# Optimization experiments

Hardware: AMD Instinct MI355X
Metric: run time of the kernel (lower is better)

The kernel has to match this reference:

```python
import jax, jax.numpy as jnp
import numpy as np

OS = 14            # output_size
GRID = 2           # ceil(roi_size/OS) = ceil(28/14) = 2 (boxes are built 28x28, sampling_ratio=-1)
NODES = OS * OS    # 196 graph nodes
EPS = 1e-5         # BatchNorm eps
K, B, C, H, W = 256, 4, 256, 112, 112


def _bn_relu(x, g, b, m, v):
    # eval-mode BatchNorm2d followed by ReLU (bn_act_conv prefix)
    s = jax.lax.rsqrt(v + EPS)
    xn = (x - m[None, :, None, None]) * s[None, :, None, None]
    return jax.nn.relu(xn * g[None, :, None, None] + b[None, :, None, None])


def _conv(x, w, b, pad):
    y = jax.lax.conv_general_dilated(x, w, (1, 1), [(pad, pad), (pad, pad)],
                                     dimension_numbers=('NCHW', 'OIHW', 'NCHW'))
    return y + b[None, :, None, None]


def _roi_align(sem, boxes):
    # torchvision roi_align, spatial_scale=1.0, aligned=False, sampling_ratio=-1 (static grid=2)
    Bs, Cc, Hh, Ww = sem.shape
    bidx = boxes[:, 0].astype(jnp.int32)
    x1, y1, x2, y2 = boxes[:, 1], boxes[:, 2], boxes[:, 3], boxes[:, 4]
    bw = jnp.maximum(x2 - x1, 1.0) / OS
    bh = jnp.maximum(y2 - y1, 1.0) / OS
    t = (jnp.arange(OS * GRID, dtype=sem.dtype) + 0.5) / GRID   # pw*GRID+ix collapsed
    xs = x1[:, None] + bw[:, None] * t                          # [K, 28]
    ys = y1[:, None] + bh[:, None] * t

    def prep(c, L):
        m = (c >= -1.0) & (c <= L)
        cc = jnp.clip(c, 0.0, L - 1)
        lo = jnp.floor(cc).astype(jnp.int32)
        hi = jnp.minimum(lo + 1, L - 1)
        return m, lo, hi, cc - lo

    my, yl, yh, ly = prep(ys, Hh)
    mx, xl, xh, lx = prep(xs, Ww)
    semt = jnp.transpose(sem, (0, 2, 3, 1))  # [B,H,W,C]

    def gat(ya, xa):
        return semt[bidx[:, None, None], ya[:, :, None], xa[:, None, :]]  # [K,28,28,C]

    ly_ = ly[:, :, None, None]
    lx_ = lx[:, None, :, None]
    val = (gat(yl, xl) * (1 - ly_) * (1 - lx_) + gat(yl, xh) * (1 - ly_) * lx_
           + gat(yh, xl) * ly_ * (1 - lx_) + gat(yh, xh) * ly_ * lx_)
    val = jnp.where((my[:, :, None] & mx[:, None, :])[..., None], val, 0.0)
    val = val.reshape(-1, OS, GRID, OS, GRID, Cc).mean(axis=(2, 4))  # avg over sampling grid
    return jnp.transpose(val, (0, 3, 1, 2))  # [K,C,14,14]


def _gcn_agg(A, x):
    # PyG gcn_norm on a fully-connected weighted graph (self loops already present):
    # deg[j] = sum_i A[i,j] (scatter on col); out[j] = sum_i d^-1/2[i] A[i,j] d^-1/2[j] x[i]
    deg = A.sum(axis=1)                 # [K,196]
    dis = jax.lax.rsqrt(deg)            # sigmoid weights > 0 => no zero degree
    Nrm = dis[:, :, None] * A * dis[:, None, :]
    return jnp.einsum('kij,kif->kjf', Nrm, x)


def _forward(roi_feature, semantic, boxes,
             bn_sem_g, bn_sem_b, bn_sem_m, bn_sem_v, conv_sem_w, conv_sem_b,
             bn_fpn_g, bn_fpn_b, bn_fpn_m, bn_fpn_v, conv_fpn_w, conv_fpn_b,
             bn_aff_g, bn_aff_b, bn_aff_m, bn_aff_v, conv_aff_w, conv_aff_b,
             gcn1_w, gcn1_b, gcn2_w, gcn2_b):
    roi_sem = _roi_align(semantic, boxes)                                   # [K,256,14,14]
    a = (_conv(_bn_relu(roi_sem, bn_sem_g, bn_sem_b, bn_sem_m, bn_sem_v), conv_sem_w, conv_sem_b, 1)
         + _conv(_bn_relu(roi_feature, bn_fpn_g, bn_fpn_b, bn_fpn_m, bn_fpn_v), conv_fpn_w, conv_fpn_b, 1))
    aff = _conv(_bn_relu(a, bn_aff_g, bn_aff_b, bn_aff_m, bn_aff_v), conv_aff_w, conv_aff_b, 0)
    A = jax.nn.sigmoid(aff.reshape(-1, NODES, NODES))                       # [K,196,196]
    X = roi_feature.reshape(-1, C, NODES).transpose(0, 2, 1)                # [K,196,256] node feats
    x1 = jax.nn.relu(_gcn_agg(A, X @ gcn1_w) + gcn1_b)                      # GCNConv(256,16)+ReLU
    x2 = _gcn_agg(A, x1 @ gcn2_w) + gcn2_b                                  # GCNConv(16,256)
    emb = x2.transpose(0, 2, 1).reshape(-1, C, OS, OS)
    return roi_sem + emb


def setup_inputs() -> dict:
    key = jax.random.key(0)
    ks = jax.random.split(key, 24)
    roi_feature = jax.random.normal(ks[0], (K, C, OS, OS), jnp.float32)
    semantic = jax.random.normal(ks[1], (B, C, H, W), jnp.float32)
    bidx = jax.random.randint(ks[2], (K,), 0, B).astype(jnp.float32)
    xy = jax.random.uniform(ks[3], (K, 2), jnp.float32, 0.0, float(H - 28))
    boxes = jnp.concatenate([bidx[:, None], xy, xy + 28.0], axis=1)  # (idx,x1,y1,x2,y2), 28x28 boxes

    def bn(kg, c):
        k1, k2, k3, k4 = jax.random.split(kg, 4)
        return (jax.random.normal(k1, (c,)) * 0.1 + 1.0,
                jax.random.normal(k2, (c,)) * 0.1,
                jax.random.normal(k3, (c,)) * 0.1,
                jax.random.uniform(k4, (c,), jnp.float32, 0.5, 1.5))
    bn_sem = bn(ks[4], C); bn_fpn = bn(ks[5], C); bn_aff = bn(ks[6], 64)
    inp = {
        'roi_feature': roi_feature, 'semantic': semantic, 'boxes': boxes,
        'bn_sem_g': bn_sem[0], 'bn_sem_b': bn_sem[1], 'bn_sem_m': bn_sem[2], 'bn_sem_v': bn_sem[3],
        'conv_sem_w': jax.random.normal(ks[7], (64, C, 3, 3)) * 0.02,
        'conv_sem_b': jax.random.normal(ks[8], (64,)) * 0.02,
        'bn_fpn_g': bn_fpn[0], 'bn_fpn_b': bn_fpn[1], 'bn_fpn_m': bn_fpn[2], 'bn_fpn_v': bn_fpn[3],
        'conv_fpn_w': jax.random.normal(ks[9], (64, C, 3, 3)) * 0.02,
        'conv_fpn_b': jax.random.normal(ks[10], (64,)) * 0.02,
        'bn_aff_g': bn_aff[0], 'bn_aff_b': bn_aff[1], 'bn_aff_m': bn_aff[2], 'bn_aff_v': bn_aff[3],
        'conv_aff_w': jax.random.normal(ks[11], (NODES, 64, 1, 1)) * 0.05,
        'conv_aff_b': jax.random.normal(ks[12], (NODES,)) * 0.05,
        'gcn1_w': jax.random.normal(ks[13], (C, 16)) * 0.05,
        'gcn1_b': jax.random.normal(ks[14], (16,)) * 0.05,
        'gcn2_w': jax.random.normal(ks[15], (16, C)) * 0.05,
        'gcn2_b': jax.random.normal(ks[16], (C,)) * 0.05,
    }
    return inp


def reference(roi_feature, semantic, boxes,
              bn_sem_g, bn_sem_b, bn_sem_m, bn_sem_v, conv_sem_w, conv_sem_b,
              bn_fpn_g, bn_fpn_b, bn_fpn_m, bn_fpn_v, conv_fpn_w, conv_fpn_b,
              bn_aff_g, bn_aff_b, bn_aff_m, bn_aff_v, conv_aff_w, conv_aff_b,
              gcn1_w, gcn1_b, gcn2_w, gcn2_b):
    return _forward(roi_feature, semantic, boxes,
                    bn_sem_g, bn_sem_b, bn_sem_m, bn_sem_v, conv_sem_w, conv_sem_b,
                    bn_fpn_g, bn_fpn_b, bn_fpn_m, bn_fpn_v, conv_fpn_w, conv_fpn_b,
                    bn_aff_g, bn_aff_b, bn_aff_m, bn_aff_v, conv_aff_w, conv_aff_b,
                    gcn1_w, gcn1_b, gcn2_w, gcn2_b)
```

## Files before the change

kernel.cpp:

```cpp
#include <hip/hip_runtime.h>
#include <hip/hip_bf16.h>

#define KBOX 256
#define CCH  256
#define NODES 196
#define OS 14

typedef __attribute__((ext_vector_type(8))) short  bf16x8;
typedef __attribute__((ext_vector_type(8))) unsigned short u16x8;
typedef __attribute__((ext_vector_type(4))) float  f32x4;
typedef __attribute__((ext_vector_type(4))) short  s16x4;
typedef __attribute__((ext_vector_type(4))) int    i32x4;

__device__ __forceinline__ short f2bf(float x) {
  __hip_bfloat16 h = __float2bfloat16(x);
  return *reinterpret_cast<short*>(&h);
}
__device__ __forceinline__ float bf2f(unsigned short u) {
  unsigned int x = ((unsigned int)u) << 16;
  union { unsigned int i; float f; } c; c.i = x;
  return c.f;
}

#define MFMA16 __builtin_amdgcn_mfma_f32_16x16x32_bf16

__global__ __launch_bounds__(256) void prep_kernel(
    const float* __restrict__ bn_sem_g, const float* __restrict__ bn_sem_b,
    const float* __restrict__ bn_sem_m, const float* __restrict__ bn_sem_v,
    const float* __restrict__ conv_sem_w, const float* __restrict__ conv_sem_b,
    const float* __restrict__ bn_fpn_g, const float* __restrict__ bn_fpn_b,
    const float* __restrict__ bn_fpn_m, const float* __restrict__ bn_fpn_v,
    const float* __restrict__ conv_fpn_w, const float* __restrict__ conv_fpn_b,
    const float* __restrict__ bn_aff_g, const float* __restrict__ bn_aff_b,
    const float* __restrict__ bn_aff_m, const float* __restrict__ bn_aff_v,
    const float* __restrict__ conv_aff_w, const float* __restrict__ g1w,
    const float* __restrict__ g2w,
    float* __restrict__ ss_sem, float* __restrict__ ss_fpn, float* __restrict__ ss_aff2,
    short* __restrict__ wfrag, short* __restrict__ wafrag, short* __restrict__ g1wf,
    short* __restrict__ g2wf)
{
  int gid = blockIdx.x * blockDim.x + threadIdx.x;
  int gsz = gridDim.x * blockDim.x;
  for (int c = gid; c < 256; c += gsz) {
    float s = bn_sem_g[c] * rsqrtf(bn_sem_v[c] + 1e-5f);
    ss_sem[c] = s; ss_sem[256 + c] = bn_sem_b[c] - bn_sem_m[c] * s;
    float s2 = bn_fpn_g[c] * rsqrtf(bn_fpn_v[c] + 1e-5f);
    ss_fpn[c] = s2; ss_fpn[256 + c] = bn_fpn_b[c] - bn_fpn_m[c] * s2;
  }
  for (int c = gid; c < 64; c += gsz) {
    float s = bn_aff_g[c] * rsqrtf(bn_aff_v[c] + 1e-5f);
    float sh = bn_aff_b[c] - bn_aff_m[c] * s;
    float bias = conv_sem_b[c] + conv_fpn_b[c];
    ss_aff2[c] = s; ss_aff2[64 + c] = bias * s + sh;
  }
  for (int idx = gid; idx < 144 * 4 * 64 * 8; idx += gsz) {
    int e = idx & 7, lane = (idx >> 3) & 63, nt = (idx >> 9) & 3, kstep = idx >> 11;
    int src = kstep / 72, rem = kstep % 72, icc = rem / 9, pos = rem % 9;
    int ky = pos / 3, kx = pos % 3;
    int oc = nt * 16 + (lane & 15);
    int ic = icc * 32 + (lane >> 4) * 8 + e;
    const float* w = src ? conv_fpn_w : conv_sem_w;
    wfrag[idx] = f2bf(w[((oc * 256 + ic) * 3 + ky) * 3 + kx]);
  }
  for (int idx = gid; idx < 2 * 13 * 64 * 8; idx += gsz) {
    int t = idx;
    int e = t & 7; t >>= 3;
    int lane = t & 63; t >>= 6;
    int nt = t % 13; int s = t / 13;
    int i = nt * 16 + (lane & 15);
    int ic = s * 32 + (lane >> 4) * 8 + e;
    wafrag[idx] = f2bf(i < NODES ? conv_aff_w[i * 64 + ic] : 0.f);
  }
  for (int idx = gid; idx < 8 * 64 * 8; idx += gsz) {
    int e = idx & 7, lane = (idx >> 3) & 63, ks = idx >> 9;
    int ic = ks * 32 + (lane >> 4) * 8 + e;
    int f = lane & 15;
    g1wf[idx] = f2bf(g1w[ic * 16 + f]);
  }
  for (int idx = gid; idx < 16 * 64 * 8; idx += gsz) {
    int e = idx & 7, lane = (idx >> 3) & 63, ct = idx >> 9;
    int kk = (lane >> 4) * 8 + e;
    int c = ct * 16 + (lane & 15);
    g2wf[idx] = f2bf(kk < 16 ? g2w[kk * 256 + c] : 0.f);
  }
}

__global__ __launch_bounds__(256) void transpose_bf16_kernel(
    const float* __restrict__ in, unsigned short* __restrict__ out, int C, int HW)
{
  __shared__ float tile[64][65];
  int nh = (HW + 63) >> 6;
  int bi = blockIdx.x;
  int cb = bi % (C >> 6); bi /= (C >> 6);
  int hb = bi % nh; int b = bi / nh;
  int tx = threadIdx.x & 63, ty = threadIdx.x >> 6;
  const float* inb = in + (size_t)b * C * HW;
  unsigned short* outb = out + (size_t)b * HW * C;
  #pragma unroll
  for (int i = ty; i < 64; i += 4) {
    int c = cb * 64 + i, hw = hb * 64 + tx;
    tile[i][tx] = (hw < HW) ? inb[(size_t)c * HW + hw] : 0.f;
  }
  __syncthreads();
  int cp = threadIdx.x & 31;
  #pragma unroll
  for (int i = (int)(threadIdx.x >> 5); i < 64; i += 8) {
    int hw = hb * 64 + i;
    if (hw < HW) {
      ushort2 v;
      v.x = (unsigned short)f2bf(tile[cp * 2][i]);
      v.y = (unsigned short)f2bf(tile[cp * 2 + 1][i]);
      *(ushort2*)&outb[(size_t)hw * C + cb * 64 + cp * 2] = v;
    }
  }
}

__global__ __launch_bounds__(512) void roi_align_kernel(
    const unsigned short* __restrict__ semt, const float* __restrict__ boxes,
    unsigned short* __restrict__ roi_sem)
{
  __shared__ unsigned short slab[5][29][256];
  int kb = blockIdx.x / 7, g = blockIdx.x % 7;
  int tid = threadIdx.x, wave = tid >> 6, lane = tid & 63;
  const float* bx = boxes + kb * 5;
  int bb = (int)bx[0];
  float x1 = bx[1], y1 = bx[2];
  float xb = x1 + 0.5f, yv = y1 + 0.5f;
  int X0 = (int)floorf(xb); float fx = xb - (float)X0;
  int Y0 = (int)floorf(yv); float fy = yv - (float)Y0;
  const unsigned short* base = semt + (size_t)bb * 12544 * 256;
  #pragma unroll
  for (int i = 0; i < 19; ++i) {
    int s = wave + i * 8;
    if (s < 145) {
      int r = s / 29, xi = s - r * 29;
      int yr = min(Y0 + 4 * g + r, 111);
      int xc = min(X0 + xi, 111);
      *(s16x4*)&slab[r][xi][lane * 4] =
          *(const s16x4*)(base + ((size_t)yr * 112 + xc) * 256 + lane * 4);
    }
  }
  __syncthreads();
  int c2 = tid & 127, grp = tid >> 7;
  int oyl = grp >> 1, og = grp & 1;
  int rb = oyl * 2;
  float w0 = 1.f - fy;
  unsigned short* op = roi_sem + (((size_t)kb * NODES) + (2 * g + oyl) * OS) * 256 + c2 * 2;
  #pragma unroll
  for (int oxs = 0; oxs < 7; ++oxs) {
    int ox = og * 7 + oxs;
    float o0 = 0.f, o1 = 0.f;
    #pragma unroll
    for (int xi = 0; xi < 3; ++xi) {
      float xw = (xi == 0) ? (1.f - fx) : (xi == 1 ? 1.f : fx);
      const unsigned short* p0 = &slab[rb][2 * ox + xi][c2 * 2];
      const unsigned short* p1 = &slab[rb + 1][2 * ox + xi][c2 * 2];
      const unsigned short* p2 = &slab[rb + 2][2 * ox + xi][c2 * 2];
      o0 += xw * (w0 * bf2f(p0[0]) + bf2f(p1[0]) + fy * bf2f(p2[0]));
      o1 += xw * (w0 * bf2f(p0[1]) + bf2f(p1[1]) + fy * bf2f(p2[1]));
    }
    ushort2 v;
    v.x = (unsigned short)f2bf(o0 * 0.25f);
    v.y = (unsigned short)f2bf(o1 * 0.25f);
    *(ushort2*)(op + (size_t)ox * 256) = v;
  }
}

__global__ __launch_bounds__(512) void conv_ab_kernel(
    const unsigned short* __restrict__ roi_sem, const unsigned short* __restrict__ roif,
    const float* __restrict__ ss_sem, const float* __restrict__ ss_fpn,
    const short* __restrict__ wfrag, const float* __restrict__ ss_aff2,
    short* __restrict__ a_rel)
{
  int k = blockIdx.x;
  int tid = threadIdx.x;
  int wave = tid >> 6, lane = tid & 63;
  int l15 = lane & 15, lq = lane >> 4;
  __shared__ short lds_in[197][40];
  __shared__ short lds_wf[18432];
  __shared__ float lds_sc[2][256], lds_sh[2][256];
  __shared__ float scA[64], cmbA[64];

  if (tid < 256) {
    lds_sc[0][tid] = ss_sem[tid]; lds_sh[0][tid] = ss_sem[256 + tid];
    lds_sc[1][tid] = ss_fpn[tid]; lds_sh[1][tid] = ss_fpn[256 + tid];
  }
  if (tid < 64) { scA[tid] = ss_aff2[tid]; cmbA[tid] = ss_aff2[64 + tid]; }
  if (tid < 40) lds_in[196][tid] = 0;

  int mt1 = wave + 8;
  int j0 = wave * 16 + l15;
  int j1 = mt1 * 16 + l15;
  int oy0 = j0 / 14, ox0 = j0 - oy0 * 14;
  int oy1 = j1 / 14, ox1 = j1 - oy1 * 14;
  bool wave_m1 = (mt1 < 13);

  u16x8 inv2[2];
  i32x4 wv[5];
  const size_t kbase = (size_t)k * NODES * CCH;

  f32x4 acc[2][4];
  #pragma unroll
  for (int i = 0; i < 2; ++i)
    #pragma unroll
    for (int j = 0; j < 4; ++j) acc[i][j] = f32x4{0.f, 0.f, 0.f, 0.f};

#define ISSUE_LOADS(P) do {                                                  \
    int src_ = (P) >> 3, icc_ = (P) & 7;                                     \
    const unsigned short* in_ = (src_ ? roif : roi_sem) + kbase + icc_ * 32; \
    inv2[0] = *(const u16x8*)(in_ + (size_t)(tid >> 2) * 256 + (tid & 3) * 8); \
    if (tid < 272) {                                                         \
      int f_ = 512 + tid;                                                    \
      inv2[1] = *(const u16x8*)(in_ + (size_t)(f_ >> 2) * 256 + (f_ & 3) * 8); \
    }                                                                        \
    const i32x4* wsl_ = (const i32x4*)(wfrag + (size_t)(src_ * 72 + icc_ * 9) * 2048); \
    _Pragma("unroll")                                                        \
    for (int i_ = 0; i_ < 4; ++i_) wv[i_] = wsl_[tid + i_ * 512];            \
    if (tid < 256) wv[4] = wsl_[2048 + tid];                                 \
  } while (0)

#define WRITE_STAGE(P) do {                                                  \
    int src_ = (P) >> 3, icc_ = (P) & 7;                                     \
    {                                                                        \
      int j_ = tid >> 2, cq_ = tid & 3;                                      \
      bf16x8 pk_;                                                            \
      _Pragma("unroll")                                                      \
      for (int u_ = 0; u_ < 8; ++u_) {                                       \
        int c_ = icc_ * 32 + cq_ * 8 + u_;                                   \
        float x_ = bf2f(inv2[0][u_]) * lds_sc[src_][c_] + lds_sh[src_][c_];  \
        pk_[u_] = f2bf(fmaxf(x_, 0.f));                                      \
      }                                                                      \
      *(bf16x8*)&lds_in[j_][cq_ * 8] = pk_;                                  \
    }                                                                        \
    if (tid < 272) {                                                         \
      int f_ = 512 + tid; int j_ = f_ >> 2, cq_ = f_ & 3;                    \
      bf16x8 pk_;                                                            \
      _Pragma("unroll")                                                      \
      for (int u_ = 0; u_ < 8; ++u_) {                                       \
        int c_ = icc_ * 32 + cq_ * 8 + u_;                                   \
        float x_ = bf2f(inv2[1][u_]) * lds_sc[src_][c_] + lds_sh[src_][c_];  \
        pk_[u_] = f2bf(fmaxf(x_, 0.f));                                      \
      }                                                                      \
      *(bf16x8*)&lds_in[j_][cq_ * 8] = pk_;                                  \
    }                                                                        \
    _Pragma("unroll")                                                        \
    for (int i_ = 0; i_ < 4; ++i_) ((i32x4*)lds_wf)[tid + i_ * 512] = wv[i_];\
    if (tid < 256) ((i32x4*)lds_wf)[2048 + tid] = wv[4];                     \
  } while (0)

  ISSUE_LOADS(0);
  __syncthreads();
  WRITE_STAGE(0);

  for (int p = 0; p < 16; ++p) {
    __syncthreads();
    if (p < 15) ISSUE_LOADS(p + 1);
    #pragma unroll
    for (int pos = 0; pos < 9; ++pos) {
      int ky = pos / 3 - 1, kx = pos % 3 - 1;
      bf16x8 bfr[4];
      #pragma unroll
      for (int n = 0; n < 4; ++n)
        bfr[n] = *(const bf16x8*)&lds_wf[((pos * 4 + n) * 64 + lane) * 8];
      {
        int ny = oy0 + ky, nx = ox0 + kx;
        bool v = ((unsigned)ny < 14u) & ((unsigned)nx < 14u);
        int np = v ? (ny * 14 + nx) : 196;
        bf16x8 afr = *(const bf16x8*)&lds_in[np][lq * 8];
        acc[0][0] = MFMA16(afr, bfr[0], acc[0][0], 0, 0, 0);
        acc[0][1] = MFMA16(afr, bfr[1], acc[0][1], 0, 0, 0);
        acc[0][2] = MFMA16(afr, bfr[2], acc[0][2], 0, 0, 0);
        acc[0][3] = MFMA16(afr, bfr[3], acc[0][3], 0, 0, 0);
      }
      if (wave_m1) {
        int ny = oy1 + ky, nx = ox1 + kx;
        bool v = (j1 < 196) & ((unsigned)ny < 14u) & ((unsigned)nx < 14u);
        int np = v ? (ny * 14 + nx) : 196;
        bf16x8 afr = *(const bf16x8*)&lds_in[np][lq * 8];
        acc[1][0] = MFMA16(afr, bfr[0], acc[1][0], 0, 0, 0);
        acc[1][1] = MFMA16(afr, bfr[1], acc[1][1], 0, 0, 0);
        acc[1][2] = MFMA16(afr, bfr[2], acc[1][2], 0, 0, 0);
        acc[1][3] = MFMA16(afr, bfr[3], acc[1][3], 0, 0, 0);
      }
    }
    __syncthreads();
    if (p < 15) WRITE_STAGE(p + 1);
  }

  #pragma unroll
  for (int mi = 0; mi < 2; ++mi) {
    int mt = wave + mi * 8;
    if (mt >= 13) continue;
    #pragma unroll
    for (int n = 0; n < 4; ++n) {
      int oc = n * 16 + l15;
      float sa = scA[oc], cb = cmbA[oc];
      #pragma unroll
      for (int r = 0; r < 4; ++r) {
        int j = mt * 16 + lq * 4 + r;
        if (j < NODES) {
          float t = fmaxf(acc[mi][n][r] * sa + cb, 0.f);
          a_rel[((size_t)k * NODES + j) * 64 + oc] = f2bf(t);
        }
      }
    }
  }
#undef ISSUE_LOADS
#undef WRITE_STAGE
}

__global__ __launch_bounds__(1024, 1) void graph_kernel(
    const short* __restrict__ a_rel, const short* __restrict__ wafrag,
    const float* __restrict__ aff_b, const short* __restrict__ g1wf,
    const float* __restrict__ g1b, const unsigned short* __restrict__ roif_bf,
    const short* __restrict__ g2wf, const float* __restrict__ g2b,
    const unsigned short* __restrict__ roi_sem, float* __restrict__ outp)
{
  __shared__ __align__(16) char smem[125840];
  const int tid = threadIdx.x, wave = tid >> 6, lane = tid & 63;
  const int l15 = lane & 15, lq = lane >> 4;
  const int k = blockIdx.x;

  char*  Ab   = smem;
  short* wa   = (short*)(smem + 96512);
  short* yfr  = (short*)(smem + 96512);
  short* zsf  = (short*)(smem + 103680);
  float* dsl  = (float*)(smem + 123136);
  float* g1bl = (float*)(smem + 123968);
  float* g2bl = (float*)(smem + 124032);
  float* affb = (float*)(smem + 125056);

  const bool wv13 = (wave < 13);
  const int jr  = wave * 16 + l15;
  const int jrc = min(jr, 195);
  const i32x4 z4 = {};

  bf16x8 af0 = {}, af1 = {};
  if (wv13) {
    const short* ap = a_rel + (size_t)k * 12544 + jrc * 64 + lq * 8;
    af0 = *(const bf16x8*)ap;
    af1 = *(const bf16x8*)(ap + 32);
  }
  {
    i32x4 w0 = ((const i32x4*)wafrag)[tid];
    i32x4 w1 = z4;
    if (tid < 640) w1 = ((const i32x4*)wafrag)[1024 + tid];
    if (tid < 832) {
      int r = tid >> 2, q = tid & 3;
      *(i32x4*)(Ab + r * 464 + 384 + q * 16) = z4;
    }
    if (tid < 196) affb[tid] = aff_b[tid];
    if (tid < 256) g2bl[tid] = g2b[tid];
    if (tid < 16)  g1bl[tid] = g1b[tid];
    ((i32x4*)wa)[tid] = w0;
    if (tid < 640) ((i32x4*)wa)[1024 + tid] = w1;
  }
  __syncthreads();

  if (wv13) {
    float rsum[4] = {0.f, 0.f, 0.f, 0.f};
    #pragma unroll
    for (int n = 0; n < 13; ++n) {
      bf16x8 b0 = *(const bf16x8*)(wa + (n * 64 + lane) * 8);
      bf16x8 b1 = *(const bf16x8*)(wa + ((13 + n) * 64 + lane) * 8);
      f32x4 acc = {0.f, 0.f, 0.f, 0.f};
      acc = MFMA16(af0, b0, acc, 0, 0, 0);
      acc = MFMA16(af1, b1, acc, 0, 0, 0);
      int i = n * 16 + l15;
      bool iv = (i < 196);
      float bv = affb[iv ? i : 0];
      #pragma unroll
      for (int r = 0; r < 4; ++r) {
        float v = acc[r] + bv;
        float s = 1.f / (1.f + __expf(-v));
        if (iv) {
          rsum[r] += s;
          *(short*)(Ab + (wave * 16 + lq * 4 + r) * 464 + i * 2) = f2bf(s);
        }
      }
    }
    #pragma unroll
    for (int r = 0; r < 4; ++r) {
      float v = rsum[r];
      v += __shfl_xor(v, 1); v += __shfl_xor(v, 2);
      v += __shfl_xor(v, 4); v += __shfl_xor(v, 8);
      int j = wave * 16 + lq * 4 + r;
      if (l15 == 0 && j < 196) dsl[j] = rsqrtf(v);
    }
  }
  __syncthreads();

  *(i32x4*)(smem + 96512 + tid * 16) = z4;
  if (tid < 256) *(i32x4*)(smem + 96512 + (1024 + tid) * 16) = z4;
  f32x4 xacc = {0.f, 0.f, 0.f, 0.f};
  if (wv13) {
    const unsigned short* Xp = roif_bf + (size_t)k * 50176 + (size_t)jrc * 256 + lq * 8;
    #pragma unroll
    for (int ks = 0; ks < 8; ++ks) {
      bf16x8 xa = *(const bf16x8*)(Xp + ks * 32);
      bf16x8 xb = *(const bf16x8*)(g1wf + (ks * 64 + lane) * 8);
      xacc = MFMA16(xa, xb, xacc, 0, 0, 0);
    }
  }
  __syncthreads();

  if (wv13) {
    #pragma unroll
    for (int r = 0; r < 4; ++r) {
      int i = wave * 16 + lq * 4 + r;
      if (i < 196) {
        float yv = dsl[i] * xacc[r];
        yfr[((i >> 5) * 64 + ((i >> 3) & 3) * 16 + l15) * 8 + (i & 7)] = f2bf(yv);
      }
    }
  }
  __syncthreads();

  f32x4 g0 = {0.f, 0.f, 0.f, 0.f};
  if (wv13) {
    #pragma unroll
    for (int ks = 0; ks < 7; ++ks) {
      bf16x8 bb = *(const bf16x8*)(yfr + (ks * 64 + lane) * 8);
      bf16x8 a0 = *(const bf16x8*)(Ab + jr * 464 + ks * 64 + lq * 16);
      g0 = MFMA16(a0, bb, g0, 0, 0, 0);
    }
  }
  __syncthreads();
  if (wv13) {
    #pragma unroll
    for (int r = 0; r < 4; ++r) {
      int i = wave * 16 + lq * 4 + r;
      if (i < 196) {
        float d = dsl[i];
        float x1v = fmaxf(g0[r] * d + g1bl[l15], 0.f);
        yfr[((i >> 5) * 64 + ((i >> 3) & 3) * 16 + l15) * 8 + (i & 7)] = f2bf(d * x1v);
      }
    }
  }
  __syncthreads();

  if (wv13) {
    f32x4 z0 = {0.f, 0.f, 0.f, 0.f};
    #pragma unroll
    for (int ks = 0; ks < 7; ++ks) {
      bf16x8 bb = *(const bf16x8*)(yfr + (ks * 64 + lane) * 8);
      bf16x8 a0 = *(const bf16x8*)(Ab + jr * 464 + ks * 64 + lq * 16);
      z0 = MFMA16(a0, bb, z0, 0, 0, 0);
    }
    #pragma unroll
    for (int r = 0; r < 4; ++r) {
      int j = wave * 16 + lq * 4 + r;
      if (j < 196) {
        float zv = z0[r] * dsl[j];
        zsf[((j >> 4) * 64 + (l15 >> 3) * 16 + (j & 15)) * 8 + (l15 & 7)] = f2bf(zv);
      }
    }
  }
  __syncthreads();

  {
    bf16x8 wf = *(const bf16x8*)(g2wf + (wave * 64 + lane) * 8);
    const unsigned short* rsmk = roi_sem + (size_t)k * 50176;
    float* op = outp + (size_t)k * 50176;
    float gbv[4];
    #pragma unroll
    for (int r = 0; r < 4; ++r) gbv[r] = g2bl[wave * 16 + lq * 4 + r];
    #pragma unroll
    for (int jt = 0; jt < 13; ++jt) {
      bf16x8 zb = *(const bf16x8*)(zsf + (jt * 64 + lane) * 8);
      f32x4 d = {0.f, 0.f, 0.f, 0.f};
      d = MFMA16(wf, zb, d, 0, 0, 0);
      int j = jt * 16 + l15;
      if (j < 196) {
        #pragma unroll
        for (int r = 0; r < 4; ++r) {
          int c = wave * 16 + lq * 4 + r;
          op[(size_t)c * 196 + j] = d[r] + gbv[r] + bf2f(rsmk[(size_t)j * 256 + c]);
        }
      }
    }
  }
}

extern "C" void kernel_launch(void* const* d_in, const int* in_sizes, int n_in,
                              void* d_out, int out_size, void* d_ws, size_t ws_size,
                              hipStream_t stream) {
  const float* roi_feature = (const float*)d_in[0];
  const float* semantic    = (const float*)d_in[1];
  const float* boxes       = (const float*)d_in[2];
  const float* bn_sem_g = (const float*)d_in[3];
  const float* bn_sem_b = (const float*)d_in[4];
  const float* bn_sem_m = (const float*)d_in[5];
  const float* bn_sem_v = (const float*)d_in[6];
  const float* conv_sem_w = (const float*)d_in[7];
  const float* conv_sem_b = (const float*)d_in[8];
  const float* bn_fpn_g = (const float*)d_in[9];
  const float* bn_fpn_b = (const float*)d_in[10];
  const float* bn_fpn_m = (const float*)d_in[11];
  const float* bn_fpn_v = (const float*)d_in[12];
  const float* conv_fpn_w = (const float*)d_in[13];
  const float* conv_fpn_b = (const float*)d_in[14];
  const float* bn_aff_g = (const float*)d_in[15];
  const float* bn_aff_b = (const float*)d_in[16];
  const float* bn_aff_m = (const float*)d_in[17];
  const float* bn_aff_v = (const float*)d_in[18];
  const float* conv_aff_w = (const float*)d_in[19];
  const float* conv_aff_b = (const float*)d_in[20];
  const float* gcn1_w = (const float*)d_in[21];
  const float* gcn1_b = (const float*)d_in[22];
  const float* gcn2_w = (const float*)d_in[23];
  const float* gcn2_b = (const float*)d_in[24];

  const size_t FT = (size_t)KBOX * NODES * CCH;
  unsigned short* ws16      = (unsigned short*)d_ws;
  unsigned short* semt_bf   = ws16;
  unsigned short* roif_bf   = semt_bf + FT;
  unsigned short* roi_sem_b = roif_bf + FT;
  short*          a_rel     = (short*)(roi_sem_b + FT);
  float*          ss_sem    = (float*)(a_rel + 3211264);
  float*          ss_fpn    = ss_sem + 512;
  float*          ss_aff2   = ss_fpn + 512;
  short*          wfrag     = (short*)(ss_aff2 + 128);
  short*          wafrag    = wfrag + 294912;
  short*          g1wf      = wafrag + 13312;
  short*          g2wf      = g1wf + 4096;

  prep_kernel<<<256, 256, 0, stream>>>(
      bn_sem_g, bn_sem_b, bn_sem_m, bn_sem_v, conv_sem_w, conv_sem_b,
      bn_fpn_g, bn_fpn_b, bn_fpn_m, bn_fpn_v, conv_fpn_w, conv_fpn_b,
      bn_aff_g, bn_aff_b, bn_aff_m, bn_aff_v, conv_aff_w, gcn1_w, gcn2_w,
      ss_sem, ss_fpn, ss_aff2, wfrag, wafrag, g1wf, g2wf);

  transpose_bf16_kernel<<<4 * 196 * 4, 256, 0, stream>>>(semantic, semt_bf, 256, 12544);
  transpose_bf16_kernel<<<4 * 4 * 256, 256, 0, stream>>>(roi_feature, roif_bf, 256, 196);
  roi_align_kernel<<<KBOX * 7, 512, 0, stream>>>(semt_bf, boxes, roi_sem_b);
  conv_ab_kernel<<<KBOX, 512, 0, stream>>>(roi_sem_b, roif_bf, ss_sem, ss_fpn, wfrag, ss_aff2, a_rel);
  graph_kernel<<<KBOX, 1024, 0, stream>>>(a_rel, wafrag, conv_aff_b, g1wf, gcn1_b, roif_bf,
                                          g2wf, gcn2_b, roi_sem_b, (float*)d_out);
}
```

Baseline: 142.3 us.

## Double-buffer conv_ab LDS stages and halve block to 256 threads

The conv_ab kernel now uses two LDS buffers for input and weight tiles, so writing stage p+1 and issuing global loads for p+2 overlap with the MFMA work on stage p. This removes one barrier per iteration. The block shrinks from 512 to 256 threads, with each wave covering up to four M tiles instead of two, which raises per-thread registers and load count. LDS use roughly doubles to about 105 KB, which may limit blocks per CU, and the grid is only 256 blocks.

```diff
diff --git a/kernel.cpp b/kernel.cpp
--- a/kernel.cpp
+++ b/kernel.cpp
@@ -166,7 +166,7 @@
   }
 }
 
-__global__ __launch_bounds__(512) void conv_ab_kernel(
+__global__ __launch_bounds__(256) void conv_ab_kernel(
     const unsigned short* __restrict__ roi_sem, const unsigned short* __restrict__ roif,
     const float* __restrict__ ss_sem, const float* __restrict__ ss_fpn,
     const short* __restrict__ wfrag, const float* __restrict__ ss_aff2,
@@ -176,120 +176,120 @@
   int tid = threadIdx.x;
   int wave = tid >> 6, lane = tid & 63;
   int l15 = lane & 15, lq = lane >> 4;
-  __shared__ short lds_in[197][40];
-  __shared__ short lds_wf[18432];
+  __shared__ short lds_in[2][197][40];
+  __shared__ short lds_wf[2][18432];
   __shared__ float lds_sc[2][256], lds_sh[2][256];
   __shared__ float scA[64], cmbA[64];
 
-  if (tid < 256) {
-    lds_sc[0][tid] = ss_sem[tid]; lds_sh[0][tid] = ss_sem[256 + tid];
-    lds_sc[1][tid] = ss_fpn[tid]; lds_sh[1][tid] = ss_fpn[256 + tid];
-  }
+  lds_sc[0][tid] = ss_sem[tid]; lds_sh[0][tid] = ss_sem[256 + tid];
+  lds_sc[1][tid] = ss_fpn[tid]; lds_sh[1][tid] = ss_fpn[256 + tid];
   if (tid < 64) { scA[tid] = ss_aff2[tid]; cmbA[tid] = ss_aff2[64 + tid]; }
-  if (tid < 40) lds_in[196][tid] = 0;
-
-  int mt1 = wave + 8;
-  int j0 = wave * 16 + l15;
-  int j1 = mt1 * 16 + l15;
-  int oy0 = j0 / 14, ox0 = j0 - oy0 * 14;
-  int oy1 = j1 / 14, ox1 = j1 - oy1 * 14;
-  bool wave_m1 = (mt1 < 13);
-
-  u16x8 inv2[2];
-  i32x4 wv[5];
+  if (tid < 40) { lds_in[0][196][tid] = 0; lds_in[1][196][tid] = 0; }
+
+  int oyA[4], oxA[4]; bool mvA[4], jvA[4];
+  #pragma unroll
+  for (int mi = 0; mi < 4; ++mi) {
+    int mt = wave + mi * 4;
+    mvA[mi] = (mt < 13);
+    int j = mt * 16 + l15;
+    jvA[mi] = (j < 196);
+    int oy = j / 14;
+    oyA[mi] = oy; oxA[mi] = j - oy * 14;
+  }
+
+  u16x8 inv[4];
+  i32x4 wv[9];
   const size_t kbase = (size_t)k * NODES * CCH;
 
-  f32x4 acc[2][4];
-  #pragma unroll
-  for (int i = 0; i < 2; ++i)
+  f32x4 acc[4][4];
+  #pragma unroll
+  for (int i = 0; i < 4; ++i)
     #pragma unroll
     for (int j = 0; j < 4; ++j) acc[i][j] = f32x4{0.f, 0.f, 0.f, 0.f};
 
 #define ISSUE_LOADS(P) do {                                                  \
     int src_ = (P) >> 3, icc_ = (P) & 7;                                     \
     const unsigned short* in_ = (src_ ? roif : roi_sem) + kbase + icc_ * 32; \
-    inv2[0] = *(const u16x8*)(in_ + (size_t)(tid >> 2) * 256 + (tid & 3) * 8); \
-    if (tid < 272) {                                                         \
-      int f_ = 512 + tid;                                                    \
-      inv2[1] = *(const u16x8*)(in_ + (size_t)(f_ >> 2) * 256 + (f_ & 3) * 8); \
+    _Pragma("unroll")                                                        \
+    for (int i_ = 0; i_ < 3; ++i_) {                                         \
+      int f_ = tid + i_ * 256;                                               \
+      inv[i_] = *(const u16x8*)(in_ + (size_t)(f_ >> 2) * 256 + (f_ & 3) * 8); \
+    }                                                                        \
+    if (tid < 16) {                                                          \
+      int f_ = 768 + tid;                                                    \
+      inv[3] = *(const u16x8*)(in_ + (size_t)(f_ >> 2) * 256 + (f_ & 3) * 8); \
     }                                                                        \
     const i32x4* wsl_ = (const i32x4*)(wfrag + (size_t)(src_ * 72 + icc_ * 9) * 2048); \
     _Pragma("unroll")                                                        \
-    for (int i_ = 0; i_ < 4; ++i_) wv[i_] = wsl_[tid + i_ * 512];            \
-    if (tid < 256) wv[4] = wsl_[2048 + tid];                                 \
+    for (int i_ = 0; i_ < 9; ++i_) wv[i_] = wsl_[tid + i_ * 256];            \
   } while (0)
 
-#define WRITE_STAGE(P) do {                                                  \
+#define WRITE_STAGE(P, BUF) do {                                             \
     int src_ = (P) >> 3, icc_ = (P) & 7;                                     \
-    {                                                                        \
-      int j_ = tid >> 2, cq_ = tid & 3;                                      \
+    _Pragma("unroll")                                                        \
+    for (int i_ = 0; i_ < 3; ++i_) {                                         \
+      int f_ = tid + i_ * 256;                                               \
+      int j_ = f_ >> 2, cq_ = f_ & 3;                                        \
       bf16x8 pk_;                                                            \
       _Pragma("unroll")                                                      \
       for (int u_ = 0; u_ < 8; ++u_) {                                       \
         int c_ = icc_ * 32 + cq_ * 8 + u_;                                   \
-        float x_ = bf2f(inv2[0][u_]) * lds_sc[src_][c_] + lds_sh[src_][c_];  \
+        float x_ = bf2f(inv[i_][u_]) * lds_sc[src_][c_] + lds_sh[src_][c_];  \
         pk_[u_] = f2bf(fmaxf(x_, 0.f));                                      \
       }                                                                      \
-      *(bf16x8*)&lds_in[j_][cq_ * 8] = pk_;                                  \
+      *(bf16x8*)&lds_in[BUF][j_][cq_ * 8] = pk_;                             \
     }                                                                        \
-    if (tid < 272) {                                                         \
-      int f_ = 512 + tid; int j_ = f_ >> 2, cq_ = f_ & 3;                    \
+    if (tid < 16) {                                                          \
+      int f_ = 768 + tid; int j_ = f_ >> 2, cq_ = f_ & 3;                    \
       bf16x8 pk_;                                                            \
       _Pragma("unroll")                                                      \
       for (int u_ = 0; u_ < 8; ++u_) {                                       \
         int c_ = icc_ * 32 + cq_ * 8 + u_;                                   \
-        float x_ = bf2f(inv2[1][u_]) * lds_sc[src_][c_] + lds_sh[src_][c_];  \
+        float x_ = bf2f(inv[3][u_]) * lds_sc[src_][c_] + lds_sh[src_][c_];   \
         pk_[u_] = f2bf(fmaxf(x_, 0.f));                                      \
       }                                                                      \
-      *(bf16x8*)&lds_in[j_][cq_ * 8] = pk_;                                  \
+      *(bf16x8*)&lds_in[BUF][j_][cq_ * 8] = pk_;                             \
     }                                                                        \
     _Pragma("unroll")                                                        \
-    for (int i_ = 0; i_ < 4; ++i_) ((i32x4*)lds_wf)[tid + i_ * 512] = wv[i_];\
-    if (tid < 256) ((i32x4*)lds_wf)[2048 + tid] = wv[4];                     \
+    for (int i_ = 0; i_ < 9; ++i_) ((i32x4*)lds_wf[BUF])[tid + i_ * 256] = wv[i_]; \
   } while (0)
 
   ISSUE_LOADS(0);
   __syncthreads();
-  WRITE_STAGE(0);
+  WRITE_STAGE(0, 0);
+  ISSUE_LOADS(1);
+  __syncthreads();
 
   for (int p = 0; p < 16; ++p) {
-    __syncthreads();
-    if (p < 15) ISSUE_LOADS(p + 1);
+    int buf = p & 1;
+    if (p < 15) WRITE_STAGE(p + 1, buf ^ 1);
+    if (p < 14) ISSUE_LOADS(p + 2);
     #pragma unroll
     for (int pos = 0; pos < 9; ++pos) {
       int ky = pos / 3 - 1, kx = pos % 3 - 1;
       bf16x8 bfr[4];
       #pragma unroll
       for (int n = 0; n < 4; ++n)
-        bfr[n] = *(const bf16x8*)&lds_wf[((pos * 4 + n) * 64 + lane) * 8];
-      {
-        int ny = oy0 + ky, nx = ox0 + kx;
-        bool v = ((unsigned)ny < 14u) & ((unsigned)nx < 14u);
+        bfr[n] = *(const bf16x8*)&lds_wf[buf][((pos * 4 + n) * 64 + lane) * 8];
+      #pragma unroll
+      for (int mi = 0; mi < 4; ++mi) {
+        if (!mvA[mi]) continue;
+        int ny = oyA[mi] + ky, nx = oxA[mi] + kx;
+        bool v = jvA[mi] & ((unsigned)ny < 14u) & ((unsigned)nx < 14u);
         int np = v ? (ny * 14 + nx) : 196;
-        bf16x8 afr = *(const bf16x8*)&lds_in[np][lq * 8];
-        acc[0][0] = MFMA16(afr, bfr[0], acc[0][0], 0, 0, 0);
-        acc[0][1] = MFMA16(afr, bfr[1], acc[0][1], 0, 0, 0);
-        acc[0][2] = MFMA16(afr, bfr[2], acc[0][2], 0, 0, 0);
-        acc[0][3] = MFMA16(afr, bfr[3], acc[0][3], 0, 0, 0);
-      }
-      if (wave_m1) {
-        int ny = oy1 + ky, nx = ox1 + kx;
-        bool v = (j1 < 196) & ((unsigned)ny < 14u) & ((unsigned)nx < 14u);
-        int np = v ? (ny * 14 + nx) : 196;
-        bf16x8 afr = *(const bf16x8*)&lds_in[np][lq * 8];
-        acc[1][0] = MFMA16(afr, bfr[0], acc[1][0], 0, 0, 0);
-        acc[1][1] = MFMA16(afr, bfr[1], acc[1][1], 0, 0, 0);
-        acc[1][2] = MFMA16(afr, bfr[2], acc[1][2], 0, 0, 0);
-        acc[1][3] = MFMA16(afr, bfr[3], acc[1][3], 0, 0, 0);
+        bf16x8 afr = *(const bf16x8*)&lds_in[buf][np][lq * 8];
+        acc[mi][0] = MFMA16(afr, bfr[0], acc[mi][0], 0, 0, 0);
+        acc[mi][1] = MFMA16(afr, bfr[1], acc[mi][1], 0, 0, 0);
+        acc[mi][2] = MFMA16(afr, bfr[2], acc[mi][2], 0, 0, 0);
+        acc[mi][3] = MFMA16(afr, bfr[3], acc[mi][3], 0, 0, 0);
       }
     }
     __syncthreads();
-    if (p < 15) WRITE_STAGE(p + 1);
-  }
-
-  #pragma unroll
-  for (int mi = 0; mi < 2; ++mi) {
-    int mt = wave + mi * 8;
+  }
+
+  #pragma unroll
+  for (int mi = 0; mi < 4; ++mi) {
+    int mt = wave + mi * 4;
     if (mt >= 13) continue;
     #pragma unroll
     for (int n = 0; n < 4; ++n) {
@@ -534,7 +534,7 @@
   transpose_bf16_kernel<<<4 * 196 * 4, 256, 0, stream>>>(semantic, semt_bf, 256, 12544);
   transpose_bf16_kernel<<<4 * 4 * 256, 256, 0, stream>>>(roi_feature, roif_bf, 256, 196);
   roi_align_kernel<<<KBOX * 7, 512, 0, stream>>>(semt_bf, boxes, roi_sem_b);
-  conv_ab_kernel<<<KBOX, 512, 0, stream>>>(roi_sem_b, roif_bf, ss_sem, ss_fpn, wfrag, ss_aff2, a_rel);
+  conv_ab_kernel<<<KBOX, 256, 0, stream>>>(roi_sem_b, roif_bf, ss_sem, ss_fpn, wfrag, ss_aff2, a_rel);
   graph_kernel<<<KBOX, 1024, 0, stream>>>(a_rel, wafrag, conv_aff_b, g1wf, gcn1_b, roif_bf,
                                           g2wf, gcn2_b, roi_sem_b, (float*)d_out);
 }
```

Result: slower. 161.5 us (+13.5%).

## Split conv_ab over semantic/fpn sources and reduce partials in graph kernel

Applied to the files above, without the earlier changes.

The conv_ab kernel now launches two blocks per box, one per input source (semantic and fpn), each covering 8 channel chunks instead of 16. The two fp32 partial sums go to a workspace, and the graph kernel adds them and applies the affinity BN+ReLU before converting to bf16. This doubles the block count from 256 to 512 to fill more CUs, at the cost of writing and re-reading fp32 partials instead of one bf16 tensor.

```diff
diff --git a/kernel.cpp b/kernel.cpp
--- a/kernel.cpp
+++ b/kernel.cpp
@@ -5,6 +5,7 @@
 #define CCH  256
 #define NODES 196
 #define OS 14
+#define FTQ 3211264
 
 typedef __attribute__((ext_vector_type(8))) short  bf16x8;
 typedef __attribute__((ext_vector_type(8))) unsigned short u16x8;
@@ -169,23 +170,21 @@
 __global__ __launch_bounds__(512) void conv_ab_kernel(
     const unsigned short* __restrict__ roi_sem, const unsigned short* __restrict__ roif,
     const float* __restrict__ ss_sem, const float* __restrict__ ss_fpn,
-    const short* __restrict__ wfrag, const float* __restrict__ ss_aff2,
-    short* __restrict__ a_rel)
+    const short* __restrict__ wfrag, float* __restrict__ a_part)
 {
-  int k = blockIdx.x;
+  int bi = blockIdx.x;
+  int k = bi >> 1, src = bi & 1;
   int tid = threadIdx.x;
   int wave = tid >> 6, lane = tid & 63;
   int l15 = lane & 15, lq = lane >> 4;
   __shared__ short lds_in[197][40];
   __shared__ short lds_wf[18432];
-  __shared__ float lds_sc[2][256], lds_sh[2][256];
-  __shared__ float scA[64], cmbA[64];
-
-  if (tid < 256) {
-    lds_sc[0][tid] = ss_sem[tid]; lds_sh[0][tid] = ss_sem[256 + tid];
-    lds_sc[1][tid] = ss_fpn[tid]; lds_sh[1][tid] = ss_fpn[256 + tid];
-  }
-  if (tid < 64) { scA[tid] = ss_aff2[tid]; cmbA[tid] = ss_aff2[64 + tid]; }
+  __shared__ float lds_sc[256], lds_sh[256];
+
+  {
+    const float* ss = src ? ss_fpn : ss_sem;
+    if (tid < 256) { lds_sc[tid] = ss[tid]; lds_sh[tid] = ss[256 + tid]; }
+  }
   if (tid < 40) lds_in[196][tid] = 0;
 
   int mt1 = wave + 8;
@@ -197,7 +196,8 @@
 
   u16x8 inv2[2];
   i32x4 wv[5];
-  const size_t kbase = (size_t)k * NODES * CCH;
+  const unsigned short* inp = (src ? roif : roi_sem) + (size_t)k * NODES * CCH;
+  const short* wbase = wfrag + (size_t)src * 72 * 2048;
 
   f32x4 acc[2][4];
   #pragma unroll
@@ -206,28 +206,28 @@
     for (int j = 0; j < 4; ++j) acc[i][j] = f32x4{0.f, 0.f, 0.f, 0.f};
 
 #define ISSUE_LOADS(P) do {                                                  \
-    int src_ = (P) >> 3, icc_ = (P) & 7;                                     \
-    const unsigned short* in_ = (src_ ? roif : roi_sem) + kbase + icc_ * 32; \
+    int icc_ = (P);                                                          \
+    const unsigned short* in_ = inp + icc_ * 32;                             \
     inv2[0] = *(const u16x8*)(in_ + (size_t)(tid >> 2) * 256 + (tid & 3) * 8); \
     if (tid < 272) {                                                         \
       int f_ = 512 + tid;                                                    \
       inv2[1] = *(const u16x8*)(in_ + (size_t)(f_ >> 2) * 256 + (f_ & 3) * 8); \
     }                                                                        \
-    const i32x4* wsl_ = (const i32x4*)(wfrag + (size_t)(src_ * 72 + icc_ * 9) * 2048); \
+    const i32x4* wsl_ = (const i32x4*)(wbase + (size_t)icc_ * 9 * 2048);     \
     _Pragma("unroll")                                                        \
     for (int i_ = 0; i_ < 4; ++i_) wv[i_] = wsl_[tid + i_ * 512];            \
     if (tid < 256) wv[4] = wsl_[2048 + tid];                                 \
   } while (0)
 
 #define WRITE_STAGE(P) do {                                                  \
-    int src_ = (P) >> 3, icc_ = (P) & 7;                                     \
+    int icc_ = (P);                                                          \
     {                                                                        \
       int j_ = tid >> 2, cq_ = tid & 3;                                      \
       bf16x8 pk_;                                                            \
       _Pragma("unroll")                                                      \
       for (int u_ = 0; u_ < 8; ++u_) {                                       \
         int c_ = icc_ * 32 + cq_ * 8 + u_;                                   \
-        float x_ = bf2f(inv2[0][u_]) * lds_sc[src_][c_] + lds_sh[src_][c_];  \
+        float x_ = bf2f(inv2[0][u_]) * lds_sc[c_] + lds_sh[c_];              \
         pk_[u_] = f2bf(fmaxf(x_, 0.f));                                      \
       }                                                                      \
       *(bf16x8*)&lds_in[j_][cq_ * 8] = pk_;                                  \
@@ -238,7 +238,7 @@
       _Pragma("unroll")                                                      \
       for (int u_ = 0; u_ < 8; ++u_) {                                       \
         int c_ = icc_ * 32 + cq_ * 8 + u_;                                   \
-        float x_ = bf2f(inv2[1][u_]) * lds_sc[src_][c_] + lds_sh[src_][c_];  \
+        float x_ = bf2f(inv2[1][u_]) * lds_sc[c_] + lds_sh[c_];              \
         pk_[u_] = f2bf(fmaxf(x_, 0.f));                                      \
       }                                                                      \
       *(bf16x8*)&lds_in[j_][cq_ * 8] = pk_;                                  \
@@ -252,9 +252,9 @@
   __syncthreads();
   WRITE_STAGE(0);
 
-  for (int p = 0; p < 16; ++p) {
+  for (int p = 0; p < 8; ++p) {
     __syncthreads();
-    if (p < 15) ISSUE_LOADS(p + 1);
+    if (p < 7) ISSUE_LOADS(p + 1);
     #pragma unroll
     for (int pos = 0; pos < 9; ++pos) {
       int ky = pos / 3 - 1, kx = pos % 3 - 1;
@@ -284,9 +284,10 @@
       }
     }
     __syncthreads();
-    if (p < 15) WRITE_STAGE(p + 1);
-  }
-
+    if (p < 7) WRITE_STAGE(p + 1);
+  }
+
+  float* op = a_part + (size_t)src * FTQ;
   #pragma unroll
   for (int mi = 0; mi < 2; ++mi) {
     int mt = wave + mi * 8;
@@ -294,14 +295,11 @@
     #pragma unroll
     for (int n = 0; n < 4; ++n) {
       int oc = n * 16 + l15;
-      float sa = scA[oc], cb = cmbA[oc];
       #pragma unroll
       for (int r = 0; r < 4; ++r) {
         int j = mt * 16 + lq * 4 + r;
-        if (j < NODES) {
-          float t = fmaxf(acc[mi][n][r] * sa + cb, 0.f);
-          a_rel[((size_t)k * NODES + j) * 64 + oc] = f2bf(t);
-        }
+        if (j < NODES)
+          op[((size_t)k * NODES + j) * 64 + oc] = acc[mi][n][r];
       }
     }
   }
@@ -310,7 +308,8 @@
 }
 
 __global__ __launch_bounds__(1024, 1) void graph_kernel(
-    const short* __restrict__ a_rel, const short* __restrict__ wafrag,
+    const float* __restrict__ a_part, const float* __restrict__ ss_aff2,
+    const short* __restrict__ wafrag,
     const float* __restrict__ aff_b, const short* __restrict__ g1wf,
     const float* __restrict__ g1b, const unsigned short* __restrict__ roif_bf,
     const short* __restrict__ g2wf, const float* __restrict__ g2b,
@@ -337,9 +336,31 @@
 
   bf16x8 af0 = {}, af1 = {};
   if (wv13) {
-    const short* ap = a_rel + (size_t)k * 12544 + jrc * 64 + lq * 8;
-    af0 = *(const bf16x8*)ap;
-    af1 = *(const bf16x8*)(ap + 32);
+    const float* p0 = a_part + ((size_t)k * NODES + jrc) * 64 + lq * 8;
+    const float* p1 = p0 + FTQ;
+    f32x4 a00 = *(const f32x4*)p0;
+    f32x4 a01 = *(const f32x4*)(p0 + 4);
+    f32x4 a02 = *(const f32x4*)(p0 + 32);
+    f32x4 a03 = *(const f32x4*)(p0 + 36);
+    f32x4 b00 = *(const f32x4*)p1;
+    f32x4 b01 = *(const f32x4*)(p1 + 4);
+    f32x4 b02 = *(const f32x4*)(p1 + 32);
+    f32x4 b03 = *(const f32x4*)(p1 + 36);
+    f32x4 sc0a = *(const f32x4*)(ss_aff2 + lq * 8);
+    f32x4 sc0b = *(const f32x4*)(ss_aff2 + lq * 8 + 4);
+    f32x4 sc1a = *(const f32x4*)(ss_aff2 + 32 + lq * 8);
+    f32x4 sc1b = *(const f32x4*)(ss_aff2 + 32 + lq * 8 + 4);
+    f32x4 sh0a = *(const f32x4*)(ss_aff2 + 64 + lq * 8);
+    f32x4 sh0b = *(const f32x4*)(ss_aff2 + 64 + lq * 8 + 4);
+    f32x4 sh1a = *(const f32x4*)(ss_aff2 + 96 + lq * 8);
+    f32x4 sh1b = *(const f32x4*)(ss_aff2 + 96 + lq * 8 + 4);
+    #pragma unroll
+    for (int e = 0; e < 4; ++e) {
+      af0[e]     = f2bf(fmaxf((a00[e] + b00[e]) * sc0a[e] + sh0a[e], 0.f));
+      af0[e + 4] = f2bf(fmaxf((a01[e] + b01[e]) * sc0b[e] + sh0b[e], 0.f));
+      af1[e]     = f2bf(fmaxf((a02[e] + b02[e]) * sc1a[e] + sh1a[e], 0.f));
+      af1[e + 4] = f2bf(fmaxf((a03[e] + b03[e]) * sc1b[e] + sh1b[e], 0.f));
+    }
   }
   {
     i32x4 w0 = ((const i32x4*)wafrag)[tid];
@@ -516,8 +537,8 @@
   unsigned short* semt_bf   = ws16;
   unsigned short* roif_bf   = semt_bf + FT;
   unsigned short* roi_sem_b = roif_bf + FT;
-  short*          a_rel     = (short*)(roi_sem_b + FT);
-  float*          ss_sem    = (float*)(a_rel + 3211264);
+  float*          a_part    = (float*)(roi_sem_b + FT);
+  float*          ss_sem    = a_part + 2 * (size_t)FTQ;
   float*          ss_fpn    = ss_sem + 512;
   float*          ss_aff2   = ss_fpn + 512;
   short*          wfrag     = (short*)(ss_aff2 + 128);
@@ -534,7 +555,7 @@
   transpose_bf16_kernel<<<4 * 196 * 4, 256, 0, stream>>>(semantic, semt_bf, 256, 12544);
   transpose_bf16_kernel<<<4 * 4 * 256, 256, 0, stream>>>(roi_feature, roif_bf, 256, 196);
   roi_align_kernel<<<KBOX * 7, 512, 0, stream>>>(semt_bf, boxes, roi_sem_b);
-  conv_ab_kernel<<<KBOX, 512, 0, stream>>>(roi_sem_b, roif_bf, ss_sem, ss_fpn, wfrag, ss_aff2, a_rel);
-  graph_kernel<<<KBOX, 1024, 0, stream>>>(a_rel, wafrag, conv_aff_b, g1wf, gcn1_b, roif_bf,
-                                          g2wf, gcn2_b, roi_sem_b, (float*)d_out);
-}
+  conv_ab_kernel<<<KBOX * 2, 512, 0, stream>>>(roi_sem_b, roif_bf, ss_sem, ss_fpn, wfrag, a_part);
+  graph_kernel<<<KBOX, 1024, 0, stream>>>(a_part, ss_aff2, wafrag, conv_aff_b, g1wf, gcn1_b,
+                                          roif_bf, g2wf, gcn2_b, roi_sem_b, (float*)d_out);
+}
```

Result: slower. 154.8 us (+8.8%).
